# Kernel tuning notes

Measured on AMD Instinct MI355X. Metric: run time of the kernel, lower is better.

## Reference

```python
import jax, jax.numpy as jnp
import numpy as np

D_MODEL = 1024
N_HEADS = 16
D_HEAD = D_MODEL // N_HEADS
CHUNK = 128
DECAY_RATE = 0.9


def setup_inputs() -> dict:
    key = jax.random.key(0)
    ks = jax.random.split(key, 10)
    B, L, D = 4, 4096, D_MODEL
    s = 1.0 / np.sqrt(D)
    return {
        "x": jax.random.normal(ks[0], (B, L, D), dtype=jnp.float32),
        "Wq": jax.random.normal(ks[1], (D, D), dtype=jnp.float32) * s,
        "bq": jnp.zeros((D,), dtype=jnp.float32),
        "Wk": jax.random.normal(ks[2], (D, D), dtype=jnp.float32) * s,
        "bk": jnp.zeros((D,), dtype=jnp.float32),
        "Wv": jax.random.normal(ks[3], (D, D), dtype=jnp.float32) * s,
        "bv": jnp.zeros((D,), dtype=jnp.float32),
        "Wo": jax.random.normal(ks[4], (D, D), dtype=jnp.float32) * s,
        "bo": jnp.zeros((D,), dtype=jnp.float32),
        "decay": jnp.full((N_HEADS,), DECAY_RATE, dtype=jnp.float32),
    }


def _retention(x, Wq, bq, Wk, bk, Wv, bv, Wo, bo, decay):
    B, L, D = x.shape
    H, Dh, C = N_HEADS, D_HEAD, CHUNK
    nC = L // C
    scale = Dh ** -0.5

    def split_heads(y):
        # [B,L,D] -> [nC, B, H, C, Dh]
        y = y.reshape(B, nC, C, H, Dh)
        return jnp.transpose(y, (1, 0, 3, 2, 4))

    q = split_heads(x @ Wq + bq)
    k = split_heads(x @ Wk + bk)
    v = split_heads(x @ Wv + bv)

    # per-head decay^position factor for query positions within a chunk: [H, C]
    pos = jnp.arange(C, dtype=jnp.float32)
    decay_fac = decay[:, None] ** pos[None, :]

    def step(carry, inp):
        pk, pv = carry            # [B,H,Dh] carried last k/v token
        qc, kc, vc = inp          # [B,H,C,Dh]
        kf = jnp.concatenate([pk[:, :, None], kc], axis=2)  # [B,H,C+1,Dh]
        vf = jnp.concatenate([pv[:, :, None], vc], axis=2)
        scores = jnp.einsum("bhqd,bhkd->bhqk", qc, kf) * scale
        scores = scores * decay_fac[None, :, :, None]
        attn = jax.nn.softmax(scores, axis=-1)
        out = jnp.einsum("bhqk,bhkd->bhqd", attn, vf)
        new_carry = (jax.lax.stop_gradient(kf[:, :, -1]),
                     jax.lax.stop_gradient(vf[:, :, -1]))
        return new_carry, out

    init = (jnp.zeros((B, H, Dh), x.dtype), jnp.zeros((B, H, Dh), x.dtype))
    _, ys = jax.lax.scan(step, init, (q, k, v))  # ys: [nC,B,H,C,Dh]
    out = jnp.transpose(ys, (1, 0, 3, 2, 4)).reshape(B, L, D)
    return out @ Wo + bo


def reference(x, Wq, bq, Wk, bk, Wv, bv, Wo, bo, decay):
    return _retention(x, Wq, bq, Wk, bk, Wv, bv, Wo, bo, decay)
```

## Files before the change

### kernel.cpp

```cpp
#include <hip/hip_runtime.h>

typedef unsigned short u16;
typedef unsigned int   u32;
typedef unsigned long long u64;

typedef __attribute__((ext_vector_type(8))) __bf16 bf16x8;
typedef __attribute__((ext_vector_type(4))) float  floatx4;

#define D_MODEL 1024
#define L_SEQ   4096
#define BATCH   4
#define N_HEADS 16
#define D_HEAD  64
#define CHUNK   128
#define N_CHUNKS 32
#define M_ROWS  (BATCH * L_SEQ)
#define NQKV    3072

__device__ __forceinline__ float bf2f(u16 u) {
    union { u32 i; float f; } x; x.i = ((u32)u) << 16; return x.f;
}
__device__ __forceinline__ u16 f2bf(float f) {
    union { u32 i; float fl; } x; x.fl = f;
    u32 i = x.i;
    u32 r = (i + 0x7FFFu + ((i >> 16) & 1u)) >> 16;
    return (u16)r;
}

__device__ __forceinline__ float load_decay(const void* dec, int h) {
    const u16* d16 = (const u16*)dec;
    const float as_bf = bf2f(d16[0]);
    if (as_bf > 1e-6f && as_bf <= 1.0001f) return bf2f(d16[h]);
    return ((const float*)dec)[h];
}

__device__ __forceinline__ void gload_lds16(const u16* g, u16* l) {
    __builtin_amdgcn_global_load_lds(
        (const __attribute__((address_space(1))) u32*)g,
        (__attribute__((address_space(3))) u32*)l, 16, 0, 0);
}

__global__ void detect_dtypes(const void* __restrict__ x,
                              const void* __restrict__ w,
                              int* __restrict__ flags) {
    const int lane = threadIdx.x;
    const u16* x16 = (const u16*)x;
    const u16* w16 = (const u16*)w;
    const float vx = fabsf(bf2f(x16[lane]));
    const float vw = fabsf(bf2f(w16[lane]));
    const bool ox = (vx != 0.0f) && (vx > 1e4f || vx < 1e-4f);
    const bool ow = (vw != 0.0f) && (vw > 1e4f || vw < 1e-4f);
    const u64 bx = __ballot(ox);
    const u64 bw = __ballot(ow);
    if (lane == 0) {
        flags[0] = (__popcll(bx) >= 8) ? 1 : 0;
        flags[1] = (__popcll(bw) >= 8) ? 1 : 0;
    }
}

__global__ __launch_bounds__(256)
void convert_x(const void* __restrict__ x, const int* __restrict__ flags,
               u16* __restrict__ xb) {
    const int mode = flags[0];
    const size_t i0 = ((size_t)blockIdx.x * 256 + threadIdx.x) * 8;
    if (mode) {
        const float* xf = (const float*)x;
        u16 tmp[8];
#pragma unroll
        for (int j = 0; j < 8; j++) tmp[j] = f2bf(xf[i0 + j]);
        *(uint4*)(xb + i0) = *(const uint4*)tmp;
    } else {
        *(uint4*)(xb + i0) = *(const uint4*)((const u16*)x + i0);
    }
}

__global__ __launch_bounds__(256)
void transpose4(const void* __restrict__ W0, const void* __restrict__ W1,
                const void* __restrict__ W2, const void* __restrict__ W3,
                const int* __restrict__ flags,
                u16* __restrict__ T0, u16* __restrict__ T1,
                u16* __restrict__ T2, u16* __restrict__ T3) {
    __shared__ u16 tile[32][33];
    const int mode = flags[1];
    const void* src; u16* dst;
    switch (blockIdx.z) {
        case 0: src = W0; dst = T0; break;
        case 1: src = W1; dst = T1; break;
        case 2: src = W2; dst = T2; break;
        default: src = W3; dst = T3; break;
    }
    const int tx = threadIdx.x & 31, ty = threadIdx.x >> 5;
    const int x0 = blockIdx.x * 32, y0 = blockIdx.y * 32;
#pragma unroll
    for (int i = 0; i < 32; i += 8) {
        const size_t idx = (size_t)(y0 + ty + i) * D_MODEL + x0 + tx;
        tile[ty + i][tx] = mode ? f2bf(((const float*)src)[idx])
                                : ((const u16*)src)[idx];
    }
    __syncthreads();
#pragma unroll
    for (int i = 0; i < 32; i += 8)
        dst[(size_t)(x0 + ty + i) * D_MODEL + y0 + tx] = tile[tx][ty + i];
}

__global__ __launch_bounds__(256)
void concat_bias(const void* __restrict__ bq, const void* __restrict__ bk,
                 const void* __restrict__ bv, const void* __restrict__ bo,
                 const int* __restrict__ flags, u16* __restrict__ dst) {
    const int i = blockIdx.x * 256 + threadIdx.x;
    const int mode = flags[1];
    const int which = i >> 10, idx = i & 1023;
    const void* src = (which == 0) ? bq : (which == 1) ? bk
                      : (which == 2) ? bv : bo;
    dst[i] = mode ? f2bf(((const float*)src)[idx]) : ((const u16*)src)[idx];
}

template <typename OutT>
__global__ __launch_bounds__(512)
void gemm_256(const u16* __restrict__ A, const u16* __restrict__ Bt,
              const u16* __restrict__ bias, OutT* __restrict__ C, int N) {
    extern __shared__ u16 lds[];
    constexpr int K  = 1024;
    constexpr int NT = K / 64;

    const int t = threadIdx.x;
    const int lane = t & 63, w = t >> 6;
    const int col16 = lane & 15, quad = lane >> 4;
    const int wm = w >> 2, wn = w & 3;

    const int nwg = gridDim.x;
    const int chunk = nwg >> 3;
    const int wg = (blockIdx.x & 7) * chunk + (blockIdx.x >> 3);
    const int m0 = (wg & 63) * 256;
    const int n0 = (wg >> 6) * 256;

    const int rl = lane >> 3;
    const int sp = lane & 7;
    const int sseg = sp ^ rl;

    auto STAGE_A = [&](int kt, int half) {
        u16* l0 = lds + (kt & 1) * 32768 + (half * 128 + w * 8) * 64;
        const u16* g0 = A + (size_t)(m0 + half * 128 + w * 8 + rl) * K
                          + kt * 64 + sseg * 8;
        gload_lds16(g0, l0);
        gload_lds16(g0 + (size_t)64 * K, l0 + 64 * 64);
    };
    auto STAGE_B = [&](int kt, int half) {
        u16* l0 = lds + (kt & 1) * 32768 + 16384 + (half * 128 + w * 8) * 64;
        const u16* g0 = Bt + (size_t)(n0 + half * 128 + w * 8 + rl) * K
                           + kt * 64 + sseg * 8;
        gload_lds16(g0, l0);
        gload_lds16(g0 + (size_t)64 * K, l0 + 64 * 64);
    };

    bf16x8 af[4][2], bfr[2][2];
    floatx4 acc[2][2][4][2];
#pragma unroll
    for (int a = 0; a < 2; a++)
#pragma unroll
        for (int b = 0; b < 2; b++)
#pragma unroll
            for (int i = 0; i < 4; i++)
#pragma unroll
                for (int j = 0; j < 2; j++)
                    acc[a][b][i][j] = floatx4{0.f, 0.f, 0.f, 0.f};

    auto LDA = [&](int cur, int mh) {
        const u16* tb = lds + cur * 32768;
        const int rbase = mh * 128 + wm * 64 + col16;
#pragma unroll
        for (int i = 0; i < 4; i++) {
            const int row = rbase + i * 16;
#pragma unroll
            for (int k0 = 0; k0 < 2; k0++) {
                const int seg = (k0 * 4 + quad) ^ (row & 7);
                af[i][k0] = *(const bf16x8*)(tb + row * 64 + seg * 8);
            }
        }
    };
    auto LDB = [&](int cur, int nh) {
        const u16* tb = lds + cur * 32768 + 16384;
        const int rbase = nh * 128 + wn * 32 + col16;
#pragma unroll
        for (int j = 0; j < 2; j++) {
            const int row = rbase + j * 16;
#pragma unroll
            for (int k0 = 0; k0 < 2; k0++) {
                const int seg = (k0 * 4 + quad) ^ (row & 7);
                bfr[j][k0] = *(const bf16x8*)(tb + row * 64 + seg * 8);
            }
        }
    };
    auto MMQ = [&](floatx4 (&aq)[4][2]) {
        __builtin_amdgcn_s_setprio(1);
#pragma unroll
        for (int i = 0; i < 4; i++)
#pragma unroll
            for (int j = 0; j < 2; j++)
#pragma unroll
                for (int k0 = 0; k0 < 2; k0++)
                    aq[i][j] = __builtin_amdgcn_mfma_f32_16x16x32_bf16(
                        af[i][k0], bfr[j][k0], aq[i][j], 0, 0, 0);
        __builtin_amdgcn_s_setprio(0);
    };

    STAGE_A(0, 0); STAGE_B(0, 0); STAGE_A(0, 1); STAGE_B(0, 1);
    STAGE_A(1, 0); STAGE_B(1, 1);
    asm volatile("s_waitcnt vmcnt(4)" ::: "memory");
    __builtin_amdgcn_s_barrier();

    for (int kt = 0; kt < NT; ++kt) {
        const int cur = kt & 1;
        LDA(cur, 0); LDB(cur, 0);
        if (kt + 1 < NT) STAGE_A(kt + 1, 1);
        __builtin_amdgcn_s_barrier();
        MMQ(acc[0][0]);
        __builtin_amdgcn_s_barrier();
        LDB(cur, 1);
        if (kt + 1 < NT) STAGE_B(kt + 1, 0);
        __builtin_amdgcn_s_barrier();
        MMQ(acc[0][1]);
        __builtin_amdgcn_s_barrier();
        LDA(cur, 1);
        if (kt + 2 < NT) STAGE_A(kt + 2, 0);
        __builtin_amdgcn_s_barrier();
        MMQ(acc[1][1]);
        __builtin_amdgcn_s_barrier();
        LDB(cur, 0);
        if (kt + 2 < NT) STAGE_B(kt + 2, 1);
        __builtin_amdgcn_s_barrier();
        MMQ(acc[1][0]);
        if (kt + 2 < NT) asm volatile("s_waitcnt vmcnt(4)" ::: "memory");
        else             asm volatile("s_waitcnt vmcnt(0)" ::: "memory");
        __builtin_amdgcn_s_barrier();
    }

    if constexpr (sizeof(OutT) == 2) {
        u16* sm = lds;
#pragma unroll
        for (int mh = 0; mh < 2; mh++) {
            __syncthreads();
#pragma unroll
            for (int nh = 0; nh < 2; nh++)
#pragma unroll
                for (int j = 0; j < 2; j++) {
                    const int lcol = nh * 128 + wn * 32 + j * 16 + col16;
                    const float bsf = bf2f(bias[n0 + lcol]);
#pragma unroll
                    for (int i = 0; i < 4; i++)
#pragma unroll
                        for (int r = 0; r < 4; r++)
                            sm[(wm * 64 + i * 16 + quad * 4 + r) * 264 + lcol] =
                                f2bf(acc[mh][nh][i][j][r] + bsf);
                }
            __syncthreads();
#pragma unroll
            for (int it = 0; it < 8; it++) {
                const int lin = it * 512 + t;
                const int row = lin >> 5, seg = lin & 31;
                *(uint4*)&C[(size_t)(m0 + mh * 128 + row) * N + n0 + seg * 8] =
                    *(const uint4*)&sm[row * 264 + seg * 8];
            }
        }
    } else {
#pragma unroll
        for (int mh = 0; mh < 2; mh++)
#pragma unroll
            for (int nh = 0; nh < 2; nh++)
#pragma unroll
                for (int j = 0; j < 2; j++) {
                    const int gcol = n0 + nh * 128 + wn * 32 + j * 16 + col16;
                    const float bsf = bf2f(bias[gcol]);
#pragma unroll
                    for (int i = 0; i < 4; i++) {
                        const int gr = m0 + mh * 128 + wm * 64 + i * 16 + quad * 4;
#pragma unroll
                        for (int r = 0; r < 4; r++)
                            C[(size_t)(gr + r) * N + gcol] =
                                acc[mh][nh][i][j][r] + bsf;
                    }
                }
    }
}

#define QS 72
#define PS 136
#define VT 136
#define KS_OFF (128 * QS)

__global__ __launch_bounds__(256)
void retention_mfma(const u16* __restrict__ qkv, const void* __restrict__ dec,
                    u16* __restrict__ att) {
    __shared__ u16 qk[2 * 128 * QS];
    __shared__ u16 vt[64 * VT];
    __shared__ float kp[64], vp[64], s0f[128];
    u16* Ps = qk;

    const int c = blockIdx.x, b = blockIdx.y, h = blockIdx.z;
    const int t = threadIdx.x;
    const int lane = t & 63, w = t >> 6;
    const int col16 = lane & 15, quad = lane >> 4;
    const int R0 = w * 32;
    const size_t base  = ((size_t)b * L_SEQ) * NQKV + h * D_HEAD;
    const size_t gbase = base + (size_t)(c * CHUNK) * NQKV;
    const size_t obase = (((size_t)b * L_SEQ) + c * CHUNK) * D_MODEL + h * D_HEAD;

#pragma unroll
    for (int it = 0; it < 4; it++) {
        const int i = it * 256 + t;
        const int row = i >> 3, seg = i & 7;
        const size_t go = gbase + (size_t)row * NQKV + seg * 8;
        *(uint4*)&qk[row * QS + seg * 8]          = *(const uint4*)(qkv + go);
        *(uint4*)&qk[KS_OFF + row * QS + seg * 8] = *(const uint4*)(qkv + go + 1024);
    }
#pragma unroll
    for (int it = 0; it < 4; it++) {
        const int i = it * 256 + t;
        const int key = i & 127, dseg = i >> 7;
        u16 tmp[8];
        *(uint4*)tmp = *(const uint4*)(qkv + gbase + (size_t)key * NQKV + 2048 + dseg * 8);
#pragma unroll
        for (int j = 0; j < 8; j++)
            vt[(dseg * 8 + j) * VT + key] = tmp[j];
    }
    if (t < 64) {
        const int gl = c * CHUNK - 1;
        float kpv = 0.f, vpv = 0.f;
        if (gl >= 0) {
            const size_t go = base + (size_t)gl * NQKV + t;
            kpv = bf2f(qkv[go + 1024]);
            vpv = bf2f(qkv[go + 2048]);
        }
        kp[t] = kpv; vp[t] = vpv;
    }
    __syncthreads();

    {
        const int row = t >> 1, half = t & 1;
        const u16* qrow = &qk[row * QS + half * 32];
        float s = 0.f;
#pragma unroll
        for (int d = 0; d < 32; d++) s += bf2f(qrow[d]) * kp[half * 32 + d];
        s += __shfl_xor(s, 1, 64);
        if (half == 0) s0f[row] = s;
    }
    __syncthreads();

    floatx4 accs[2][8];
#pragma unroll
    for (int rt = 0; rt < 2; rt++)
#pragma unroll
        for (int ct = 0; ct < 8; ct++)
            accs[rt][ct] = floatx4{0.f, 0.f, 0.f, 0.f};

#pragma unroll
    for (int k0 = 0; k0 < 2; k0++) {
        bf16x8 af0 = *(const bf16x8*)&qk[(R0 + col16) * QS + k0 * 32 + quad * 8];
        bf16x8 af1 = *(const bf16x8*)&qk[(R0 + 16 + col16) * QS + k0 * 32 + quad * 8];
#pragma unroll
        for (int ct = 0; ct < 8; ct++) {
            bf16x8 bfr = *(const bf16x8*)&qk[KS_OFF + (ct * 16 + col16) * QS + k0 * 32 + quad * 8];
            accs[0][ct] = __builtin_amdgcn_mfma_f32_16x16x32_bf16(af0, bfr, accs[0][ct], 0, 0, 0);
            accs[1][ct] = __builtin_amdgcn_mfma_f32_16x16x32_bf16(af1, bfr, accs[1][ct], 0, 0, 0);
        }
    }
    __syncthreads();

    const float dval = load_decay(dec, h);
    const float logd = __logf(dval);
    float p0v[2][4], invv[2][4];
#pragma unroll
    for (int rt = 0; rt < 2; rt++) {
#pragma unroll
        for (int r = 0; r < 4; r++) {
            const int row = R0 + rt * 16 + quad * 4 + r;
            const float dp = __expf((float)row * logd) * 0.125f;
            const float s0p = s0f[row] * dp;
            float vals[8];
            float vmax = s0p;
#pragma unroll
            for (int ct = 0; ct < 8; ct++) {
                vals[ct] = accs[rt][ct][r] * dp;
                vmax = fmaxf(vmax, vals[ct]);
            }
#pragma unroll
            for (int off = 1; off < 16; off <<= 1)
                vmax = fmaxf(vmax, __shfl_xor(vmax, off, 64));
            float lsum = 0.f;
#pragma unroll
            for (int ct = 0; ct < 8; ct++) {
                const float e = __expf(vals[ct] - vmax);
                lsum += e;
                Ps[row * PS + ct * 16 + col16] = f2bf(e);
            }
#pragma unroll
            for (int off = 1; off < 16; off <<= 1)
                lsum += __shfl_xor(lsum, off, 64);
            const float p0 = __expf(s0p - vmax);
            p0v[rt][r] = p0;
            invv[rt][r] = 1.0f / (lsum + p0);
        }
    }

    floatx4 acco[2][4];
#pragma unroll
    for (int rt = 0; rt < 2; rt++)
#pragma unroll
        for (int nt = 0; nt < 4; nt++)
            acco[rt][nt] = floatx4{0.f, 0.f, 0.f, 0.f};

#pragma unroll
    for (int k0 = 0; k0 < 4; k0++) {
        bf16x8 af0 = *(const bf16x8*)&Ps[(R0 + col16) * PS + k0 * 32 + quad * 8];
        bf16x8 af1 = *(const bf16x8*)&Ps[(R0 + 16 + col16) * PS + k0 * 32 + quad * 8];
#pragma unroll
        for (int nt = 0; nt < 4; nt++) {
            bf16x8 bfr = *(const bf16x8*)&vt[(nt * 16 + col16) * VT + k0 * 32 + quad * 8];
            acco[0][nt] = __builtin_amdgcn_mfma_f32_16x16x32_bf16(af0, bfr, acco[0][nt], 0, 0, 0);
            acco[1][nt] = __builtin_amdgcn_mfma_f32_16x16x32_bf16(af1, bfr, acco[1][nt], 0, 0, 0);
        }
    }

#pragma unroll
    for (int nt = 0; nt < 4; nt++) {
        const int gcol = nt * 16 + col16;
        const float vpc = vp[gcol];
#pragma unroll
        for (int rt = 0; rt < 2; rt++) {
#pragma unroll
            for (int r = 0; r < 4; r++) {
                const int row = R0 + rt * 16 + quad * 4 + r;
                const float val = (acco[rt][nt][r] + p0v[rt][r] * vpc) * invv[rt][r];
                att[obase + (size_t)row * D_MODEL + gcol] = f2bf(val);
            }
        }
    }
}

extern "C" void kernel_launch(void* const* d_in, const int* in_sizes, int n_in,
                              void* d_out, int out_size, void* d_ws, size_t ws_size,
                              hipStream_t stream) {
    const void* x   = d_in[0];
    const void* Wq  = d_in[1];
    const void* bq  = d_in[2];
    const void* Wk  = d_in[3];
    const void* bk  = d_in[4];
    const void* Wv  = d_in[5];
    const void* bv  = d_in[6];
    const void* Wo  = d_in[7];
    const void* bo  = d_in[8];
    const void* dec = d_in[9];
    float* out = (float*)d_out;

    char* ws = (char*)d_ws;
    const size_t mat = (size_t)M_ROWS * D_MODEL * sizeof(u16);
    const size_t wsz = (size_t)D_MODEL * D_MODEL * sizeof(u16);
    u16* xb   = (u16*)(ws);
    u16* qkv  = (u16*)(ws + mat);
    u16* WT   = (u16*)(ws + 4 * mat);
    u16* WoT  = WT + 3 * (size_t)D_MODEL * D_MODEL;
    u16* bias = (u16*)(ws + 4 * mat + 4 * wsz);
    int* flags = (int*)(ws + 4 * mat + 4 * wsz + 8192);

    dim3 tb(256);
    detect_dtypes<<<1, 64, 0, stream>>>(x, Wq, flags);
    convert_x<<<8192, tb, 0, stream>>>(x, flags, xb);
    transpose4<<<dim3(32, 32, 4), tb, 0, stream>>>(
        Wq, Wk, Wv, Wo, flags,
        WT, WT + wsz / 2, WT + wsz, WoT);
    concat_bias<<<16, tb, 0, stream>>>(bq, bk, bv, bo, flags, bias);
    gemm_256<u16><<<dim3(64 * 12), dim3(512), 131072, stream>>>(
        xb, WT, bias, qkv, NQKV);
    retention_mfma<<<dim3(N_CHUNKS, BATCH, N_HEADS), tb, 0, stream>>>(qkv, dec, xb);
    gemm_256<float><<<dim3(64 * 4), dim3(512), 131072, stream>>>(
        xb, WoT, bias + 3072, out, D_MODEL);
}
```

Baseline: 349.3 us.

## Switch GEMM to 32x32x16 MFMA tiles, drop mid-iteration barriers, simplify WG swizzle

Replaces the 16x16x32 bf16 MFMA fragments in the 256x256 GEMM with 32x32x16 instructions, so each wave issues fewer, larger MFMAs and does fewer LDS fragment loads per unit of compute. It also removes the barrier after each MMQ phase in the K loop and changes the workgroup-to-tile mapping to a fixed 8x8 swizzle that no longer depends on grid size. Removing barriers risks LDS read/write races between fragment loads and the async stages into the same buffer. The fixed swizzle assumes 64 M tiles and a grid that is a multiple of 64.

```diff
diff --git a/kernel.cpp b/kernel.cpp
--- a/kernel.cpp
+++ b/kernel.cpp
@@ -6,6 +6,7 @@
 
 typedef __attribute__((ext_vector_type(8))) __bf16 bf16x8;
 typedef __attribute__((ext_vector_type(4))) float  floatx4;
+typedef __attribute__((ext_vector_type(16))) float floatx16;
 
 #define D_MODEL 1024
 #define L_SEQ   4096
@@ -125,18 +126,15 @@
 
     const int t = threadIdx.x;
     const int lane = t & 63, w = t >> 6;
-    const int col16 = lane & 15, quad = lane >> 4;
+    const int l31 = lane & 31, hi = lane >> 5;
     const int wm = w >> 2, wn = w & 3;
 
-    const int nwg = gridDim.x;
-    const int chunk = nwg >> 3;
-    const int wg = (blockIdx.x & 7) * chunk + (blockIdx.x >> 3);
-    const int m0 = (wg & 63) * 256;
-    const int n0 = (wg >> 6) * 256;
+    const int bid = blockIdx.x;
+    const int m0 = (((bid & 7) << 3) + ((bid >> 3) & 7)) * 256;
+    const int n0 = (bid >> 6) * 256;
 
     const int rl = lane >> 3;
-    const int sp = lane & 7;
-    const int sseg = sp ^ rl;
+    const int sseg = (lane & 7) ^ rl;
 
     auto STAGE_A = [&](int kt, int half) {
         u16* l0 = lds + (kt & 1) * 32768 + (half * 128 + w * 8) * 64;
@@ -153,54 +151,47 @@
         gload_lds16(g0 + (size_t)64 * K, l0 + 64 * 64);
     };
 
-    bf16x8 af[4][2], bfr[2][2];
-    floatx4 acc[2][2][4][2];
+    bf16x8 af[2][4], bfr[4];
+    floatx16 acc[2][2][2];
 #pragma unroll
     for (int a = 0; a < 2; a++)
 #pragma unroll
         for (int b = 0; b < 2; b++)
 #pragma unroll
-            for (int i = 0; i < 4; i++)
-#pragma unroll
-                for (int j = 0; j < 2; j++)
-                    acc[a][b][i][j] = floatx4{0.f, 0.f, 0.f, 0.f};
+            for (int i = 0; i < 2; i++)
+#pragma unroll
+                for (int r = 0; r < 16; r++)
+                    acc[a][b][i][r] = 0.f;
 
     auto LDA = [&](int cur, int mh) {
         const u16* tb = lds + cur * 32768;
-        const int rbase = mh * 128 + wm * 64 + col16;
-#pragma unroll
-        for (int i = 0; i < 4; i++) {
-            const int row = rbase + i * 16;
-#pragma unroll
-            for (int k0 = 0; k0 < 2; k0++) {
-                const int seg = (k0 * 4 + quad) ^ (row & 7);
-                af[i][k0] = *(const bf16x8*)(tb + row * 64 + seg * 8);
+#pragma unroll
+        for (int i = 0; i < 2; i++) {
+            const int row = mh * 128 + wm * 64 + i * 32 + l31;
+#pragma unroll
+            for (int ks = 0; ks < 4; ks++) {
+                const int seg = (ks * 2 + hi) ^ (row & 7);
+                af[i][ks] = *(const bf16x8*)(tb + row * 64 + seg * 8);
             }
         }
     };
     auto LDB = [&](int cur, int nh) {
         const u16* tb = lds + cur * 32768 + 16384;
-        const int rbase = nh * 128 + wn * 32 + col16;
-#pragma unroll
-        for (int j = 0; j < 2; j++) {
-            const int row = rbase + j * 16;
-#pragma unroll
-            for (int k0 = 0; k0 < 2; k0++) {
-                const int seg = (k0 * 4 + quad) ^ (row & 7);
-                bfr[j][k0] = *(const bf16x8*)(tb + row * 64 + seg * 8);
-            }
+        const int row = nh * 128 + wn * 32 + l31;
+#pragma unroll
+        for (int ks = 0; ks < 4; ks++) {
+            const int seg = (ks * 2 + hi) ^ (row & 7);
+            bfr[ks] = *(const bf16x8*)(tb + row * 64 + seg * 8);
         }
     };
-    auto MMQ = [&](floatx4 (&aq)[4][2]) {
+    auto MMQ = [&](floatx16 (&aq)[2]) {
         __builtin_amdgcn_s_setprio(1);
 #pragma unroll
-        for (int i = 0; i < 4; i++)
-#pragma unroll
-            for (int j = 0; j < 2; j++)
-#pragma unroll
-                for (int k0 = 0; k0 < 2; k0++)
-                    aq[i][j] = __builtin_amdgcn_mfma_f32_16x16x32_bf16(
-                        af[i][k0], bfr[j][k0], aq[i][j], 0, 0, 0);
+        for (int i = 0; i < 2; i++)
+#pragma unroll
+            for (int ks = 0; ks < 4; ks++)
+                aq[i] = __builtin_amdgcn_mfma_f32_32x32x16_bf16(
+                    af[i][ks], bfr[ks], aq[i], 0, 0, 0);
         __builtin_amdgcn_s_setprio(0);
     };
 
@@ -215,17 +206,14 @@
         if (kt + 1 < NT) STAGE_A(kt + 1, 1);
         __builtin_amdgcn_s_barrier();
         MMQ(acc[0][0]);
-        __builtin_amdgcn_s_barrier();
         LDB(cur, 1);
         if (kt + 1 < NT) STAGE_B(kt + 1, 0);
         __builtin_amdgcn_s_barrier();
         MMQ(acc[0][1]);
-        __builtin_amdgcn_s_barrier();
         LDA(cur, 1);
         if (kt + 2 < NT) STAGE_A(kt + 2, 0);
         __builtin_amdgcn_s_barrier();
         MMQ(acc[1][1]);
-        __builtin_amdgcn_s_barrier();
         LDB(cur, 0);
         if (kt + 2 < NT) STAGE_B(kt + 2, 1);
         __builtin_amdgcn_s_barrier();
@@ -241,18 +229,18 @@
         for (int mh = 0; mh < 2; mh++) {
             __syncthreads();
 #pragma unroll
-            for (int nh = 0; nh < 2; nh++)
-#pragma unroll
-                for (int j = 0; j < 2; j++) {
-                    const int lcol = nh * 128 + wn * 32 + j * 16 + col16;
-                    const float bsf = bf2f(bias[n0 + lcol]);
-#pragma unroll
-                    for (int i = 0; i < 4; i++)
-#pragma unroll
-                        for (int r = 0; r < 4; r++)
-                            sm[(wm * 64 + i * 16 + quad * 4 + r) * 264 + lcol] =
-                                f2bf(acc[mh][nh][i][j][r] + bsf);
-                }
+            for (int nh = 0; nh < 2; nh++) {
+                const int lcol = nh * 128 + wn * 32 + l31;
+                const float bsf = bf2f(bias[n0 + lcol]);
+#pragma unroll
+                for (int i = 0; i < 2; i++)
+#pragma unroll
+                    for (int r = 0; r < 16; r++) {
+                        const int srow = wm * 64 + i * 32 +
+                                         (r & 3) + 8 * (r >> 2) + 4 * hi;
+                        sm[srow * 264 + lcol] = f2bf(acc[mh][nh][i][r] + bsf);
+                    }
+            }
             __syncthreads();
 #pragma unroll
             for (int it = 0; it < 8; it++) {
@@ -266,20 +254,18 @@
 #pragma unroll
         for (int mh = 0; mh < 2; mh++)
 #pragma unroll
-            for (int nh = 0; nh < 2; nh++)
-#pragma unroll
-                for (int j = 0; j < 2; j++) {
-                    const int gcol = n0 + nh * 128 + wn * 32 + j * 16 + col16;
-                    const float bsf = bf2f(bias[gcol]);
-#pragma unroll
-                    for (int i = 0; i < 4; i++) {
-                        const int gr = m0 + mh * 128 + wm * 64 + i * 16 + quad * 4;
-#pragma unroll
-                        for (int r = 0; r < 4; r++)
-                            C[(size_t)(gr + r) * N + gcol] =
-                                acc[mh][nh][i][j][r] + bsf;
+            for (int nh = 0; nh < 2; nh++) {
+                const int gcol = n0 + nh * 128 + wn * 32 + l31;
+                const float bsf = bf2f(bias[gcol]);
+#pragma unroll
+                for (int i = 0; i < 2; i++)
+#pragma unroll
+                    for (int r = 0; r < 16; r++) {
+                        const int gr = m0 + mh * 128 + wm * 64 + i * 32 +
+                                       (r & 3) + 8 * (r >> 2) + 4 * hi;
+                        C[(size_t)gr * N + gcol] = acc[mh][nh][i][r] + bsf;
                     }
-                }
+            }
     }
 }
 
```

Result: faster. 335.2 us (-4.1%).

## Double-buffer register fragments and reschedule GEMM main loop to overlap LDS reads with MFMA

Applied to the files above, without the earlier changes.

Reworks the 256x256 GEMM main loop to keep two sets of A/B register fragments. LDS reads for the next quadrant now issue before the current quadrant's MFMA block, and fewer barriers are used per k-step. It also changes the global-to-LDS staging order, unrolls the loop by 2, adds a min-blocks hint to launch_bounds, and replaces the chunked workgroup swizzle with a simpler bid-based mapping. The aim is to hide LDS and global latency behind matrix-core work, at the cost of more register pressure and a more delicate vmcnt/barrier schedule.

```diff
diff --git a/kernel.cpp b/kernel.cpp
--- a/kernel.cpp
+++ b/kernel.cpp
@@ -116,7 +116,7 @@
 }
 
 template <typename OutT>
-__global__ __launch_bounds__(512)
+__global__ __launch_bounds__(512, 2)
 void gemm_256(const u16* __restrict__ A, const u16* __restrict__ Bt,
               const u16* __restrict__ bias, OutT* __restrict__ C, int N) {
     extern __shared__ u16 lds[];
@@ -128,32 +128,23 @@
     const int col16 = lane & 15, quad = lane >> 4;
     const int wm = w >> 2, wn = w & 3;
 
-    const int nwg = gridDim.x;
-    const int chunk = nwg >> 3;
-    const int wg = (blockIdx.x & 7) * chunk + (blockIdx.x >> 3);
-    const int m0 = (wg & 63) * 256;
-    const int n0 = (wg >> 6) * 256;
+    const int bid = blockIdx.x;
+    const int m0 = (((bid & 7) << 3) + ((bid >> 3) & 7)) * 256;
+    const int n0 = (bid >> 6) * 256;
 
     const int rl = lane >> 3;
-    const int sp = lane & 7;
-    const int sseg = sp ^ rl;
-
-    auto STAGE_A = [&](int kt, int half) {
-        u16* l0 = lds + (kt & 1) * 32768 + (half * 128 + w * 8) * 64;
-        const u16* g0 = A + (size_t)(m0 + half * 128 + w * 8 + rl) * K
+    const int sseg = (lane & 7) ^ rl;
+
+    auto STAGE = [&](const u16* __restrict__ G, int kt, int isB, int half) {
+        u16* l0 = lds + (kt & 1) * 32768 + isB * 16384
+                      + (half * 128 + w * 8) * 64;
+        const u16* g0 = G + (size_t)((isB ? n0 : m0) + half * 128 + w * 8 + rl) * K
                           + kt * 64 + sseg * 8;
         gload_lds16(g0, l0);
         gload_lds16(g0 + (size_t)64 * K, l0 + 64 * 64);
     };
-    auto STAGE_B = [&](int kt, int half) {
-        u16* l0 = lds + (kt & 1) * 32768 + 16384 + (half * 128 + w * 8) * 64;
-        const u16* g0 = Bt + (size_t)(n0 + half * 128 + w * 8 + rl) * K
-                           + kt * 64 + sseg * 8;
-        gload_lds16(g0, l0);
-        gload_lds16(g0 + (size_t)64 * K, l0 + 64 * 64);
-    };
-
-    bf16x8 af[4][2], bfr[2][2];
+
+    bf16x8 af0[4][2], af1[4][2], bb0[2][2], bb1[2][2];
     floatx4 acc[2][2][4][2];
 #pragma unroll
     for (int a = 0; a < 2; a++)
@@ -165,12 +156,11 @@
                 for (int j = 0; j < 2; j++)
                     acc[a][b][i][j] = floatx4{0.f, 0.f, 0.f, 0.f};
 
-    auto LDA = [&](int cur, int mh) {
-        const u16* tb = lds + cur * 32768;
-        const int rbase = mh * 128 + wm * 64 + col16;
+    auto LDA = [&](bf16x8 (&af)[4][2], int kt, int mh) {
+        const u16* tb = lds + (kt & 1) * 32768;
 #pragma unroll
         for (int i = 0; i < 4; i++) {
-            const int row = rbase + i * 16;
+            const int row = mh * 128 + wm * 64 + i * 16 + col16;
 #pragma unroll
             for (int k0 = 0; k0 < 2; k0++) {
                 const int seg = (k0 * 4 + quad) ^ (row & 7);
@@ -178,62 +168,63 @@
             }
         }
     };
-    auto LDB = [&](int cur, int nh) {
-        const u16* tb = lds + cur * 32768 + 16384;
-        const int rbase = nh * 128 + wn * 32 + col16;
+    auto LDB = [&](bf16x8 (&bb)[2][2], int kt, int nh) {
+        const u16* tb = lds + (kt & 1) * 32768 + 16384;
 #pragma unroll
         for (int j = 0; j < 2; j++) {
-            const int row = rbase + j * 16;
+            const int row = nh * 128 + wn * 32 + j * 16 + col16;
 #pragma unroll
             for (int k0 = 0; k0 < 2; k0++) {
                 const int seg = (k0 * 4 + quad) ^ (row & 7);
-                bfr[j][k0] = *(const bf16x8*)(tb + row * 64 + seg * 8);
+                bb[j][k0] = *(const bf16x8*)(tb + row * 64 + seg * 8);
             }
         }
     };
-    auto MMQ = [&](floatx4 (&aq)[4][2]) {
-        __builtin_amdgcn_s_setprio(1);
-#pragma unroll
-        for (int i = 0; i < 4; i++)
-#pragma unroll
-            for (int j = 0; j < 2; j++)
-#pragma unroll
-                for (int k0 = 0; k0 < 2; k0++)
-                    aq[i][j] = __builtin_amdgcn_mfma_f32_16x16x32_bf16(
-                        af[i][k0], bfr[j][k0], aq[i][j], 0, 0, 0);
-        __builtin_amdgcn_s_setprio(0);
-    };
-
-    STAGE_A(0, 0); STAGE_B(0, 0); STAGE_A(0, 1); STAGE_B(0, 1);
-    STAGE_A(1, 0); STAGE_B(1, 1);
-    asm volatile("s_waitcnt vmcnt(4)" ::: "memory");
+
+#define MMQ(MH, NH, AF, BB)                                                   \
+    do {                                                                      \
+        __builtin_amdgcn_s_setprio(1);                                        \
+        _Pragma("unroll")                                                     \
+        for (int i = 0; i < 4; i++)                                           \
+            _Pragma("unroll")                                                 \
+            for (int j = 0; j < 2; j++)                                       \
+                _Pragma("unroll")                                             \
+                for (int k0 = 0; k0 < 2; k0++)                                \
+                    acc[MH][NH][i][j] =                                       \
+                        __builtin_amdgcn_mfma_f32_16x16x32_bf16(              \
+                            AF[i][k0], BB[j][k0], acc[MH][NH][i][j], 0, 0, 0);\
+        __builtin_amdgcn_s_setprio(0);                                        \
+    } while (0)
+
+    STAGE(A, 0, 0, 0); STAGE(Bt, 0, 1, 0); STAGE(A, 0, 0, 1); STAGE(Bt, 0, 1, 1);
+    STAGE(A, 1, 0, 0); STAGE(Bt, 1, 1, 0); STAGE(A, 1, 0, 1);
+    asm volatile("s_waitcnt vmcnt(8)" ::: "memory");
     __builtin_amdgcn_s_barrier();
-
+    LDA(af0, 0, 0); LDB(bb0, 0, 0);
+
+#pragma unroll 2
     for (int kt = 0; kt < NT; ++kt) {
-        const int cur = kt & 1;
-        LDA(cur, 0); LDB(cur, 0);
-        if (kt + 1 < NT) STAGE_A(kt + 1, 1);
-        __builtin_amdgcn_s_barrier();
-        MMQ(acc[0][0]);
-        __builtin_amdgcn_s_barrier();
-        LDB(cur, 1);
-        if (kt + 1 < NT) STAGE_B(kt + 1, 0);
-        __builtin_amdgcn_s_barrier();
-        MMQ(acc[0][1]);
-        __builtin_amdgcn_s_barrier();
-        LDA(cur, 1);
-        if (kt + 2 < NT) STAGE_A(kt + 2, 0);
-        __builtin_amdgcn_s_barrier();
-        MMQ(acc[1][1]);
-        __builtin_amdgcn_s_barrier();
-        LDB(cur, 0);
-        if (kt + 2 < NT) STAGE_B(kt + 2, 1);
-        __builtin_amdgcn_s_barrier();
-        MMQ(acc[1][0]);
-        if (kt + 2 < NT) asm volatile("s_waitcnt vmcnt(4)" ::: "memory");
+        if (kt + 1 < NT) STAGE(Bt, kt + 1, 1, 1);
+        if (kt + 1 < NT) asm volatile("s_waitcnt vmcnt(8)" ::: "memory");
         else             asm volatile("s_waitcnt vmcnt(0)" ::: "memory");
         __builtin_amdgcn_s_barrier();
-    }
+        LDB(bb1, kt, 1);
+        MMQ(0, 0, af0, bb0);
+        if (kt + 2 < NT) STAGE(A, kt + 2, 0, 0);
+        __builtin_amdgcn_s_barrier();
+        LDA(af1, kt, 1);
+        MMQ(0, 1, af0, bb1);
+        if (kt + 2 < NT) STAGE(Bt, kt + 2, 1, 0);
+        if (kt + 2 < NT)      asm volatile("s_waitcnt vmcnt(8)" ::: "memory");
+        else if (kt + 2 == NT) asm volatile("s_waitcnt vmcnt(4)" ::: "memory");
+        __builtin_amdgcn_s_barrier();
+        MMQ(1, 0, af1, bb0);
+        if (kt + 2 < NT) STAGE(A, kt + 2, 0, 1);
+        __builtin_amdgcn_s_barrier();
+        if (kt + 1 < NT) { LDA(af0, kt + 1, 0); LDB(bb0, kt + 1, 0); }
+        MMQ(1, 1, af1, bb1);
+    }
+#undef MMQ
 
     if constexpr (sizeof(OutT) == 2) {
         u16* sm = lds;
```

Result: slower. 359.0 us (+2.8%).
